# Kernel optimization log

Measured on AMD Instinct MI355X. Metric: run time of the kernel, lower is better.

The kernel has to match this reference:

```python
import jax, jax.numpy as jnp
import numpy as np

K = 3  # kernel_size per dim
DIM = 3
NUM_K = K ** DIM  # 27
# the 2^3 corner offsets of the linear B-spline support
OFFS = np.array([[(s >> d) & 1 for d in range(DIM)] for s in range(2 ** DIM)], dtype=np.int32)  # [8,3]
STRIDES = np.array([K ** d for d in range(DIM)], dtype=np.int32)  # [1,3,9]


def bspline_basis(pseudo):
    """Open B-spline basis, degree 1. pseudo: [E,3] in [0,1]. Returns basis [E,8], kidx [E,8]."""
    v = pseudo * (K - 1)
    i0 = jnp.clip(jnp.floor(v), 0, K - 2)
    f = v - i0  # fractional part in [0,1]
    i0 = i0.astype(jnp.int32)
    offs = jnp.asarray(OFFS)  # [8,3]
    w = jnp.where(offs[None].astype(bool), f[:, None, :], 1.0 - f[:, None, :])  # [E,8,3]
    basis = jnp.prod(w, axis=-1)  # [E,8]
    kidx = jnp.sum((i0[:, None, :] + offs[None]) * jnp.asarray(STRIDES)[None, None, :], axis=-1)  # [E,8]
    return basis, kidx


def spline_conv(x, src, dst, pseudo, W, Wroot, b, num_nodes):
    """SplineConv (degree 1, mean aggregation, root weight + bias)."""
    cout = W.shape[-1]
    xW = jnp.einsum('nc,kco->nko', x, W)  # [N,27,Cout]
    basis, kidx = bspline_basis(pseudo)
    flat = src[:, None] * NUM_K + kidx  # [E,8]
    g = xW.reshape(-1, cout)[flat]  # [E,8,Cout] -- dominant gather
    msg = jnp.einsum('es,eso->eo', basis, g)  # [E,Cout]
    agg = jax.ops.segment_sum(msg, dst, num_segments=num_nodes)
    cnt = jax.ops.segment_sum(jnp.ones((src.shape[0],), x.dtype), dst, num_segments=num_nodes)
    return agg / jnp.maximum(cnt, 1.0)[:, None] + x @ Wroot + b


def seg_max(x, seg, num_segments):
    m = jax.ops.segment_max(x, seg, num_segments=num_segments)
    return jnp.where(jnp.isfinite(m), m, 0.0)  # empty clusters -> 0


def setup_inputs() -> dict:
    key = jax.random.key(0)
    ks = jax.random.split(key, 16)
    N, E, B = 80000, 1280000, 16
    N1, N2 = N // 2, N1 if False else (N // 2) // 2  # N1=40000, N2=20000
    N1 = N // 2
    N2 = N1 // 2
    x = jax.random.normal(ks[0], (N, 2), dtype=jnp.float32)
    edge_index = jax.random.randint(ks[1], (2, E), 0, N, dtype=jnp.int32)
    edge_attr = jax.random.uniform(ks[2], (E, 3), dtype=jnp.float32)
    batch = jnp.sort(jax.random.randint(ks[3], (N,), 0, B, dtype=jnp.int32))
    cluster1 = jax.random.randint(ks[4], (N,), 0, N1, dtype=jnp.int32)
    cluster2 = jax.random.randint(ks[5], (N1,), 0, N2, dtype=jnp.int32)
    W1 = jax.random.normal(ks[6], (NUM_K, 2, 8), dtype=jnp.float32) * 0.3
    root1 = jax.random.normal(ks[7], (2, 8), dtype=jnp.float32) * 0.3
    b1 = jnp.zeros((8,), jnp.float32)
    W2 = jax.random.normal(ks[8], (NUM_K, 8, 16), dtype=jnp.float32) * 0.2
    root2 = jax.random.normal(ks[9], (8, 16), dtype=jnp.float32) * 0.2
    b2 = jnp.zeros((16,), jnp.float32)
    fc1_w = jax.random.normal(ks[10], (16, 64), dtype=jnp.float32) * 0.2
    fc1_b = jnp.zeros((64,), jnp.float32)
    fc2_w = jax.random.normal(ks[11], (64, 1), dtype=jnp.float32) * 0.2
    fc2_b = jnp.zeros((1,), jnp.float32)
    return dict(x=x, edge_index=edge_index, edge_attr=edge_attr, batch=batch,
                cluster1=cluster1, cluster2=cluster2,
                W1=W1, root1=root1, b1=b1, W2=W2, root2=root2, b2=b2,
                fc1_w=fc1_w, fc1_b=fc1_b, fc2_w=fc2_w, fc2_b=fc2_b)


def reference(x, edge_index, edge_attr, batch, cluster1, cluster2,
              W1, root1, b1, W2, root2, b2, fc1_w, fc1_b, fc2_w, fc2_b):
    N = x.shape[0]
    N1 = cluster1.max() * 0 + cluster2.shape[0]  # static: 40000
    N1 = cluster2.shape[0]
    N2 = N1 // 2
    B = 16
    src, dst = edge_index[0], edge_index[1]
    # level 1: SplineConv + ELU
    h = jax.nn.elu(spline_conv(x, src, dst, edge_attr, W1, root1, b1, N))
    # max_pool with precomputed cluster assignment (replaces graclus)
    x1 = seg_max(h, cluster1, N1)
    batch1 = jnp.maximum(jax.ops.segment_max(batch, cluster1, num_segments=N1), 0)
    src2 = cluster1[src]
    dst2 = cluster1[dst]
    # level 2: SplineConv + ELU on coarsened graph
    h2 = jax.nn.elu(spline_conv(x1, src2, dst2, edge_attr, W2, root2, b2, N1))
    x2 = seg_max(h2, cluster2, N2)
    batch2 = jnp.maximum(jax.ops.segment_max(batch1, cluster2, num_segments=N2), 0)
    # scatter_mean over graphs
    s = jax.ops.segment_sum(x2, batch2, num_segments=B)
    c = jax.ops.segment_sum(jnp.ones((N2,), x.dtype), batch2, num_segments=B)
    g = s / jnp.maximum(c, 1.0)[:, None]  # [B,16]
    g = jax.nn.elu(g @ fc1_w + fc1_b)  # dropout is identity in eval mode
    return jax.nn.elu(g @ fc2_w + fc2_b)  # [B,1]
```

## Files before the change

### kernel.cpp

```cpp
#include <hip/hip_runtime.h>
#include <hip/hip_fp16.h>
#include <math.h>


__device__ __forceinline__ float eluf(float x) {
    return x > 0.f ? x : (expf(x) - 1.f);
}

__device__ __forceinline__ float hlo(int v) {
    __half2 h; *(int*)&h = v; return __low2float(h);
}
__device__ __forceinline__ float hhi(int v) {
    __half2 h; *(int*)&h = v; return __high2float(h);
}

typedef _Float16 half2v __attribute__((ext_vector_type(2)));

__device__ __forceinline__ half2v uash2(unsigned u) {
    half2v h; *(unsigned*)&h = u; return h;
}

__device__ __forceinline__ float dot2f(half2v a, half2v b, float c) {
#if __has_builtin(__builtin_amdgcn_fdot2)
    return __builtin_amdgcn_fdot2(a, b, c, false);
#else
    return c + (float)a[0] * (float)b[0] + (float)a[1] * (float)b[1];
#endif
}

#define W1_STRIDE 20
#define W2H_STRIDE 68


__global__ __launch_bounds__(256) void hist_kernel(
    const int* __restrict__ ei, const int* __restrict__ cluster1,
    const int* __restrict__ cluster2,
    int* __restrict__ deg, int* __restrict__ rank,
    int* __restrict__ cdeg, int* __restrict__ rankC,
    int* __restrict__ c2deg, int* __restrict__ rank2,
    int E, int N, int N1)
{
    int i = blockIdx.x * 256 + threadIdx.x;
    if (i < E)  rank[i]  = atomicAdd(&deg[ei[E + i]], 1);
    if (i < N)  rankC[i] = atomicAdd(&cdeg[cluster1[i]], 1);
    if (i < N1) rank2[i] = atomicAdd(&c2deg[cluster2[i]], 1);
}

#define SCAN_CHUNK 4096

__global__ __launch_bounds__(256) void scan_one(
    const int* __restrict__ in0, int* __restrict__ out0, int* __restrict__ st0, int L0, int nb0,
    const int* __restrict__ in1, int* __restrict__ out1, int* __restrict__ st1, int L1, int nb1,
    const int* __restrict__ in2, int* __restrict__ out2, int* __restrict__ st2, int L2)
{
    int b = blockIdx.x;
    const int* in; int* out; int* st; int L;
    if (b < nb0)            { in = in0; out = out0; st = st0; L = L0; }
    else if (b < nb0 + nb1) { b -= nb0; in = in1; out = out1; st = st1; L = L1; }
    else                    { b -= nb0 + nb1; in = in2; out = out2; st = st2; L = L2; }
    int nb = (L + SCAN_CHUNK - 1) / SCAN_CHUNK;

    __shared__ int ls[256];
    __shared__ int pre[32];
    __shared__ int blkExcl;
    int t = threadIdx.x;
    int base = b * SCAN_CHUNK + t * 16;
    int v[16];
    int s = 0;
#pragma unroll
    for (int j = 0; j < 16; ++j) {
        int val = (base + j < L) ? in[base + j] : 0;
        v[j] = s;
        s += val;
    }
    ls[t] = s;
    __syncthreads();
    for (int off = 1; off < 256; off <<= 1) {
        int tv = (t >= off) ? ls[t - off] : 0;
        __syncthreads();
        ls[t] += tv;
        __syncthreads();
    }
    int excl = ls[t] - s;
    int total = ls[255];
    if (t == 255) {
        __threadfence();
        atomicExch(&st[b], total + 1);
    }
    if (t < b) {
        int val;
        do { val = atomicAdd(&st[t], 0); } while (val == 0);
        pre[t] = val - 1;
    }
    __syncthreads();
    if (t == 0) {
        int r = 0;
        for (int j = 0; j < b; ++j) r += pre[j];
        blkExcl = r;
    }
    __syncthreads();
    int be = blkExcl;
#pragma unroll
    for (int j = 0; j < 16; ++j)
        if (base + j < L) out[base + j] = be + excl + v[j];
    if (b == nb - 1 && t == 255) out[L] = be + total;
}

__global__ __launch_bounds__(256) void scatB_kernel(
    const int* __restrict__ ei, const float* __restrict__ attr,
    const int* __restrict__ cluster1, const int* __restrict__ cluster2,
    const float2* __restrict__ x, const float* __restrict__ W1,
    const int* __restrict__ doffs, const int* __restrict__ rank,
    const int* __restrict__ coff, const int* __restrict__ rankC,
    const int* __restrict__ c2off, const int* __restrict__ rank2,
    int* __restrict__ nidx, int* __restrict__ n1idx,
    int4* __restrict__ rec4, int E, int N, int N1)
{
    __shared__ float lw[27 * W1_STRIDE];
    for (int i = threadIdx.x; i < 27 * 16; i += 256)
        lw[(i >> 4) * W1_STRIDE + (i & 15)] = W1[i];
    __syncthreads();

    int i = blockIdx.x * 256 + threadIdx.x;
    if (i < E) {
        int s = ei[i], d = ei[E + i];
        int p = doffs[d] + rank[i];

        float vx = attr[3 * i] * 2.f, vy = attr[3 * i + 1] * 2.f, vz = attr[3 * i + 2] * 2.f;
        float ix = fmaxf(fminf(floorf(vx), 1.f), 0.f);
        float iy = fmaxf(fminf(floorf(vy), 1.f), 0.f);
        float iz = fmaxf(fminf(floorf(vz), 1.f), 0.f);
        float fx = vx - ix, fy = vy - iy, fz = vz - iz;
        int ibase = (int)ix + 3 * (int)iy + 9 * (int)iz;

        float2 xv = x[s];
        float wxv[2] = {1.f - fx, fx}, wyv[2] = {1.f - fy, fy}, wzv[2] = {1.f - fz, fz};
        float m[8];
#pragma unroll
        for (int o = 0; o < 8; ++o) m[o] = 0.f;
#pragma unroll
        for (int j = 0; j < 8; ++j) {
            int cx = j & 1, cy = (j >> 1) & 1, cz = j >> 2;
            float w = wxv[cx] * wyv[cy] * wzv[cz];
            const float* Wk = &lw[(ibase + cx + 3 * cy + 9 * cz) * W1_STRIDE];
            float a = w * xv.x, bb = w * xv.y;
            const float4 wa0 = *(const float4*)&Wk[0];
            const float4 wa1 = *(const float4*)&Wk[4];
            const float4 wb0 = *(const float4*)&Wk[8];
            const float4 wb1 = *(const float4*)&Wk[12];
            m[0] += a * wa0.x + bb * wb0.x;
            m[1] += a * wa0.y + bb * wb0.y;
            m[2] += a * wa0.z + bb * wb0.z;
            m[3] += a * wa0.w + bb * wb0.w;
            m[4] += a * wa1.x + bb * wb1.x;
            m[5] += a * wa1.y + bb * wb1.y;
            m[6] += a * wa1.z + bb * wb1.z;
            m[7] += a * wa1.w + bb * wb1.w;
        }

        unsigned hfx = __half_as_ushort(__float2half_rn(fx));
        unsigned hfy = __half_as_ushort(__float2half_rn(fy));
        unsigned hfz = __half_as_ushort(__float2half_rn(fz));
        int s2 = cluster1[s];
        int4 ra = make_int4(s2 | (ibase << 16),
                            (int)(hfx | (hfy << 16)), (int)hfz, d);
        __half2 h01 = __floats2half2_rn(m[0], m[1]);
        __half2 h23 = __floats2half2_rn(m[2], m[3]);
        __half2 h45 = __floats2half2_rn(m[4], m[5]);
        __half2 h67 = __floats2half2_rn(m[6], m[7]);
        int4 rb = make_int4(*(int*)&h01, *(int*)&h23, *(int*)&h45, *(int*)&h67);
        rec4[2 * (size_t)p]     = ra;
        rec4[2 * (size_t)p + 1] = rb;
    }
    if (i < N)  nidx[coff[cluster1[i]] + rankC[i]] = i;
    if (i < N1) n1idx[c2off[cluster2[i]] + rank2[i]] = i;
}

__global__ __launch_bounds__(256) void reduce1_kernel(
    const int* __restrict__ doffs, const unsigned short* __restrict__ recU,
    float* __restrict__ M1, int N)
{
    int lane = threadIdx.x & 63;
    int ch = lane & 7, q = lane >> 3;
    int d = (blockIdx.x << 2) + (threadIdx.x >> 6);
    if (d >= N) return;
    int beg = doffs[d], end = doffs[d + 1];
    float acc = 0.f;
    for (int p = beg + q; p < end; p += 8)
        acc += __half2float(__ushort_as_half(recU[(size_t)p * 16 + 8 + ch]));
    acc += __shfl_xor(acc, 8);
    acc += __shfl_xor(acc, 16);
    acc += __shfl_xor(acc, 32);
    if (q == 0)
        M1[(size_t)d * 8 + ch] = acc / fmaxf((float)(end - beg), 1.f);
}

__global__ __launch_bounds__(256) void node1_kernel(
    const int* __restrict__ coff, const int* __restrict__ nidx,
    const float* __restrict__ M1, const float2* __restrict__ x,
    const float* __restrict__ root1, const float* __restrict__ b1,
    const int* __restrict__ batch,
    float* __restrict__ x1c, unsigned short* __restrict__ x1chU,
    int* __restrict__ batch1, int N1)
{
    int t = blockIdx.x * 256 + threadIdx.x;
    if (t >= N1 * 8) return;
    int c = t >> 3, ch = t & 7;
    int cb = coff[c], ce = coff[c + 1];
    float r0 = root1[ch], r1 = root1[8 + ch], bo = b1[ch];
    float hm = -INFINITY;
    int bm = 0;
    for (int idx = cb; idx < ce; ++idx) {
        int d = nidx[idx];
        float2 xv = x[d];
        float h = eluf(M1[d * 8 + ch] + xv.x * r0 + xv.y * r1 + bo);
        hm = fmaxf(hm, h);
        bm = max(bm, batch[d]);
    }
    if (ce == cb) hm = 0.f;
    x1c[t] = hm;
    x1chU[t] = __half_as_ushort(__float2half_rn(hm));
    if (ch == 0) batch1[c] = bm;
}

__global__ __launch_bounds__(256) void edge2m_kernel(
    const int4* __restrict__ rec4, const unsigned short* __restrict__ x1chU,
    const float* __restrict__ W2, unsigned short* __restrict__ msg2h, int E)
{
    __shared__ unsigned lwh[27 * W2H_STRIDE];
    for (int i = threadIdx.x; i < 27 * 64; i += 256) {
        int k = i >> 6, r = i & 63;
        int o = r >> 2, c2 = r & 3;
        float a = W2[(k * 8 + 2 * c2) * 16 + o];
        float b = W2[(k * 8 + 2 * c2 + 1) * 16 + o];
        __half2 h = __floats2half2_rn(a, b);
        lwh[k * W2H_STRIDE + r] = *(unsigned*)&h;
    }
    __syncthreads();

    int t = blockIdx.x * 256 + threadIdx.x;
    if (t >= E * 4) return;
    int p = t >> 2, oq = t & 3;
    int4 m = rec4[2 * (size_t)p];
    int s2 = m.x & 0xFFFF;
    int ibase = (m.x >> 16) & 31;
    float fx = hlo(m.y), fy = hhi(m.y), fz = hlo(m.z);

    const uint4 xv4 = *(const uint4*)&x1chU[(size_t)s2 * 8];
    half2v xh0 = uash2(xv4.x), xh1 = uash2(xv4.y),
           xh2 = uash2(xv4.z), xh3 = uash2(xv4.w);

    float wx0 = 1.f - fx, wy0 = 1.f - fy, wz0 = 1.f - fz;
    float acc0 = 0.f, acc1 = 0.f, acc2 = 0.f, acc3 = 0.f;
#pragma unroll
    for (int j = 0; j < 8; ++j) {
        int cx = j & 1, cy = (j >> 1) & 1, cz = j >> 2;
        float w = (cx ? fx : wx0) * (cy ? fy : wy0) * (cz ? fz : wz0);
        int k = ibase + cx + 3 * cy + 9 * cz;
        const unsigned* base = &lwh[k * W2H_STRIDE + oq * 16];
        uint4 v0 = *(const uint4*)(base);
        uint4 v1 = *(const uint4*)(base + 4);
        uint4 v2 = *(const uint4*)(base + 8);
        uint4 v3 = *(const uint4*)(base + 12);
        float s0 = dot2f(xh0, uash2(v0.x), dot2f(xh1, uash2(v0.y),
                   dot2f(xh2, uash2(v0.z), dot2f(xh3, uash2(v0.w), 0.f))));
        float s1 = dot2f(xh0, uash2(v1.x), dot2f(xh1, uash2(v1.y),
                   dot2f(xh2, uash2(v1.z), dot2f(xh3, uash2(v1.w), 0.f))));
        float s2v = dot2f(xh0, uash2(v2.x), dot2f(xh1, uash2(v2.y),
                    dot2f(xh2, uash2(v2.z), dot2f(xh3, uash2(v2.w), 0.f))));
        float s3 = dot2f(xh0, uash2(v3.x), dot2f(xh1, uash2(v3.y),
                   dot2f(xh2, uash2(v3.z), dot2f(xh3, uash2(v3.w), 0.f))));
        acc0 = fmaf(w, s0, acc0);
        acc1 = fmaf(w, s1, acc1);
        acc2 = fmaf(w, s2v, acc2);
        acc3 = fmaf(w, s3, acc3);
    }
    __half2 lo = __floats2half2_rn(acc0, acc1);
    __half2 hi = __floats2half2_rn(acc2, acc3);
    uint2 outv = make_uint2(*(unsigned*)&lo, *(unsigned*)&hi);
    *(uint2*)&msg2h[(size_t)p * 16 + oq * 4] = outv;
}

__global__ __launch_bounds__(256) void reduce2_kernel(
    const int* __restrict__ coff, const int* __restrict__ nidx,
    const int* __restrict__ doffs, const unsigned short* __restrict__ msg2h,
    float* __restrict__ M2, int N1)
{
    int lane = threadIdx.x & 63;
    int o = lane & 15, q = lane >> 4;
    int c = (blockIdx.x << 2) + (threadIdx.x >> 6);
    if (c >= N1) return;
    int cb = coff[c], ce = coff[c + 1];
    float acc = 0.f;
    int cnt = 0;
    for (int idx = cb; idx < ce; ++idx) {
        int d = nidx[idx];
        int beg = doffs[d], end = doffs[d + 1];
        cnt += end - beg;
        for (int p = beg + q; p < end; p += 4)
            acc += __half2float(__ushort_as_half(msg2h[(size_t)p * 16 + o]));
    }
    acc += __shfl_xor(acc, 16);
    acc += __shfl_xor(acc, 32);
    if (q == 0) M2[(size_t)c * 16 + o] = acc / fmaxf((float)cnt, 1.f);
}

__global__ __launch_bounds__(256) void node2_kernel(
    const int* __restrict__ c2off, const int* __restrict__ n1idx,
    const float* __restrict__ M2, const float* __restrict__ x1c,
    const float* __restrict__ root2, const float* __restrict__ b2,
    const int* __restrict__ batch1,
    float* __restrict__ gsum, float* __restrict__ gcnt, int N2)
{
    __shared__ float ls[16 * 16];
    __shared__ float lc[16];
    for (int i = threadIdx.x; i < 256; i += 256) ls[i] = 0.f;
    if (threadIdx.x < 16) lc[threadIdx.x] = 0.f;
    __syncthreads();

    int c2 = blockIdx.x * 256 + threadIdx.x;
    if (c2 < N2) {
        int cb = c2off[c2], ce = c2off[c2 + 1];
        float hm[16];
#pragma unroll
        for (int o = 0; o < 16; ++o) hm[o] = -INFINITY;
        int bm = 0;
        for (int idx = cb; idx < ce; ++idx) {
            int n1 = n1idx[idx];
            const float4* xr4 = (const float4*)&x1c[(size_t)n1 * 8];
            float4 xa = xr4[0], xb = xr4[1];
            float xr[8] = {xa.x, xa.y, xa.z, xa.w, xb.x, xb.y, xb.z, xb.w};
#pragma unroll
            for (int o = 0; o < 16; ++o) {
                float v = M2[(size_t)n1 * 16 + o] + b2[o];
#pragma unroll
                for (int c8 = 0; c8 < 8; ++c8) v += xr[c8] * root2[c8 * 16 + o];
                hm[o] = fmaxf(hm[o], eluf(v));
            }
            bm = max(bm, batch1[n1]);
        }
        if (ce == cb) {
#pragma unroll
            for (int o = 0; o < 16; ++o) hm[o] = 0.f;
        }
#pragma unroll
        for (int o = 0; o < 16; ++o) atomicAdd(&ls[bm * 16 + o], hm[o]);
        atomicAdd(&lc[bm], 1.f);
    }
    __syncthreads();
    for (int i = threadIdx.x; i < 256; i += 256) unsafeAtomicAdd(&gsum[i], ls[i]);
    if (threadIdx.x < 16) unsafeAtomicAdd(&gcnt[threadIdx.x], lc[threadIdx.x]);
}

__global__ __launch_bounds__(256) void head_kernel(
    const float* __restrict__ gsum, const float* __restrict__ gcnt,
    const float* __restrict__ fc1_w, const float* __restrict__ fc1_b,
    const float* __restrict__ fc2_w, const float* __restrict__ fc2_b,
    float* __restrict__ out, int B)
{
    __shared__ float g[16 * 16];
    __shared__ float h1[16 * 64];
    int t = threadIdx.x;
    if (t < B * 16) {
        int b = t >> 4;
        g[t] = gsum[t] / fmaxf(gcnt[b], 1.f);
    }
    __syncthreads();
    for (int j = t; j < B * 64; j += 256) {
        int b = j >> 6, jj = j & 63;
        float s = fc1_b[jj];
#pragma unroll
        for (int c = 0; c < 16; ++c) s += g[b * 16 + c] * fc1_w[c * 64 + jj];
        h1[j] = eluf(s);
    }
    __syncthreads();
    if (t < B) {
        float s = fc2_b[0];
#pragma unroll
        for (int j = 0; j < 64; ++j) s += h1[t * 64 + j] * fc2_w[j];
        out[t] = eluf(s);
    }
}

extern "C" void kernel_launch(void* const* d_in, const int* in_sizes, int n_in,
                              void* d_out, int out_size, void* d_ws, size_t ws_size,
                              hipStream_t stream)
{
    const float* x        = (const float*)d_in[0];
    const int*   ei       = (const int*)  d_in[1];
    const float* attr     = (const float*)d_in[2];
    const int*   batch    = (const int*)  d_in[3];
    const int*   cluster1 = (const int*)  d_in[4];
    const int*   cluster2 = (const int*)  d_in[5];
    const float* W1       = (const float*)d_in[6];
    const float* root1    = (const float*)d_in[7];
    const float* b1       = (const float*)d_in[8];
    const float* W2       = (const float*)d_in[9];
    const float* root2    = (const float*)d_in[10];
    const float* b2       = (const float*)d_in[11];
    const float* fc1_w    = (const float*)d_in[12];
    const float* fc1_b    = (const float*)d_in[13];
    const float* fc2_w    = (const float*)d_in[14];
    const float* fc2_b    = (const float*)d_in[15];

    const int N  = in_sizes[0] / 2;
    const int E  = in_sizes[1] / 2;
    const int N1 = in_sizes[5];
    const int N2 = N1 / 2;
    const int B  = out_size;

    const int nb0 = (N  + SCAN_CHUNK - 1) / SCAN_CHUNK;
    const int nb1 = (N1 + SCAN_CHUNK - 1) / SCAN_CHUNK;
    const int nb2 = (N2 + SCAN_CHUNK - 1) / SCAN_CHUNK;

    int* wi = (int*)d_ws;
    size_t off = 0;
    auto alloc = [&](size_t n, size_t align = 1) {
        off = (off + align - 1) & ~(align - 1);
        size_t r = off; off += n; return r;
    };
    int*   deg    = wi + alloc(N);
    int*   cdeg   = wi + alloc(N1);
    int*   c2deg  = wi + alloc(N2);
    float* gsum   = (float*)(wi + alloc((size_t)B * 16));
    float* gcnt   = (float*)(wi + alloc(B));
    int*   st0    = wi + alloc(32);
    int*   st1    = wi + alloc(32);
    int*   st2    = wi + alloc(32);
    const size_t zcount = off;
    int*   doffs  = wi + alloc(N + 1);
    int*   coff   = wi + alloc(N1 + 1);
    int*   c2off  = wi + alloc(N2 + 1);
    int*   rank   = wi + alloc(E);
    int*   rankC  = wi + alloc(N);
    int*   rank2  = wi + alloc(N1);
    int*   nidx   = wi + alloc(N);
    int*   n1idx  = wi + alloc(N1);
    int4*  rec4   = (int4*)(wi + alloc((size_t)E * 8, 8));
    unsigned short* msg2h = (unsigned short*)(wi + alloc((size_t)E * 8, 4));
    float* M1     = (float*)(wi + alloc((size_t)N * 8, 4));
    float* x1c    = (float*)(wi + alloc((size_t)N1 * 8, 4));
    unsigned short* x1chU = (unsigned short*)(wi + alloc((size_t)N1 * 4, 4));
    int*   batch1 = wi + alloc(N1);
    float* M2     = (float*)(wi + alloc((size_t)N1 * 16, 4));
    (void)ws_size;

    hipMemsetAsync(d_ws, 0, zcount * sizeof(int), stream);

    const int eb = (E + 255) / 256;
    hist_kernel<<<eb, 256, 0, stream>>>(ei, cluster1, cluster2,
                                        deg, rank, cdeg, rankC, c2deg, rank2, E, N, N1);
    scan_one<<<nb0 + nb1 + nb2, 256, 0, stream>>>(deg, doffs, st0, N, nb0,
                                                  cdeg, coff, st1, N1, nb1,
                                                  c2deg, c2off, st2, N2);
    scatB_kernel<<<eb, 256, 0, stream>>>(ei, attr, cluster1, cluster2,
                                         (const float2*)x, W1,
                                         doffs, rank, coff, rankC, c2off, rank2,
                                         nidx, n1idx, rec4, E, N, N1);
    reduce1_kernel<<<(N + 3) / 4, 256, 0, stream>>>(
        doffs, (const unsigned short*)rec4, M1, N);
    node1_kernel<<<(N1 * 8 + 255) / 256, 256, 0, stream>>>(
        coff, nidx, M1, (const float2*)x, root1, b1, batch,
        x1c, x1chU, batch1, N1);
    edge2m_kernel<<<(E * 4 + 255) / 256, 256, 0, stream>>>(
        rec4, x1chU, W2, msg2h, E);
    reduce2_kernel<<<(N1 + 3) / 4, 256, 0, stream>>>(
        coff, nidx, doffs, msg2h, M2, N1);
    node2_kernel<<<(N2 + 255) / 256, 256, 0, stream>>>(
        c2off, n1idx, M2, x1c, root2, b2, batch1, gsum, gcnt, N2);
    head_kernel<<<1, 256, 0, stream>>>(gsum, gcnt, fc1_w, fc1_b, fc2_w, fc2_b,
                                       (float*)d_out, B);
}
```

Measured before the change: 347.9 us.

## Accumulate basis-weighted inputs per node before applying W2, dropping per-edge messages

The level-2 spline conv now reorders the algebra. Each destination node accumulates the basis-weighted source features into a 27x8 vector Y in registers and shared memory, then multiplies by W2 once per node, instead of computing a 16-wide message per edge. This removes the per-edge msg2h buffer write and reread, and most of the per-edge dot products. The cost is per-edge work spread over 64 lanes with mostly zero weights, plus a new per-node intermediate M2n. A separate comb2 kernel averages M2n per cluster, and node2 is reworked to one thread per output channel with root2 staged in shared memory.

```diff
diff --git a/kernel.cpp b/kernel.cpp
--- a/kernel.cpp
+++ b/kernel.cpp
@@ -14,22 +14,15 @@
     __half2 h; *(int*)&h = v; return __high2float(h);
 }
 
-typedef _Float16 half2v __attribute__((ext_vector_type(2)));
-
-__device__ __forceinline__ half2v uash2(unsigned u) {
-    half2v h; *(unsigned*)&h = u; return h;
-}
-
-__device__ __forceinline__ float dot2f(half2v a, half2v b, float c) {
-#if __has_builtin(__builtin_amdgcn_fdot2)
-    return __builtin_amdgcn_fdot2(a, b, c, false);
-#else
-    return c + (float)a[0] * (float)b[0] + (float)a[1] * (float)b[1];
-#endif
+__device__ __forceinline__ float hlou(unsigned v) {
+    __half2 h; *(unsigned*)&h = v; return __low2float(h);
+}
+__device__ __forceinline__ float hhiu(unsigned v) {
+    __half2 h; *(unsigned*)&h = v; return __high2float(h);
 }
 
 #define W1_STRIDE 20
-#define W2H_STRIDE 68
+#define W2T_STRIDE 217
 
 
 __global__ __launch_bounds__(256) void hist_kernel(
@@ -223,89 +216,93 @@
     if (ch == 0) batch1[c] = bm;
 }
 
-__global__ __launch_bounds__(256) void edge2m_kernel(
-    const int4* __restrict__ rec4, const unsigned short* __restrict__ x1chU,
-    const float* __restrict__ W2, unsigned short* __restrict__ msg2h, int E)
-{
-    __shared__ unsigned lwh[27 * W2H_STRIDE];
-    for (int i = threadIdx.x; i < 27 * 64; i += 256) {
-        int k = i >> 6, r = i & 63;
-        int o = r >> 2, c2 = r & 3;
-        float a = W2[(k * 8 + 2 * c2) * 16 + o];
-        float b = W2[(k * 8 + 2 * c2 + 1) * 16 + o];
-        __half2 h = __floats2half2_rn(a, b);
-        lwh[k * W2H_STRIDE + r] = *(unsigned*)&h;
-    }
-    __syncthreads();
-
+__global__ __launch_bounds__(256) void edge2Y_kernel(
+    const int* __restrict__ doffs, const int4* __restrict__ rec4,
+    const unsigned short* __restrict__ x1chU, const float* __restrict__ W2,
+    float* __restrict__ M2n, int N)
+{
+    __shared__ float w2t[16 * W2T_STRIDE];
+    __shared__ float Y[4 * 256];
+    int tid = threadIdx.x;
+    for (int j = tid; j < 27 * 8 * 16; j += 256) {
+        int o = j & 15, kc = j >> 4;
+        w2t[o * W2T_STRIDE + kc] = W2[j];
+    }
+    int wid = tid >> 6, lane = tid & 63;
+    int d = (blockIdx.x << 2) + wid;
+    float* Yw = &Y[wid * 256];
+
+    int myk = lane >> 1;
+    int csel = lane & 1;
+    float y0 = 0.f, y1 = 0.f, y2 = 0.f, y3 = 0.f;
+    if (d < N) {
+        int beg = doffs[d], end = doffs[d + 1];
+        for (int p = beg; p < end; ++p) {
+            int4 ra = rec4[2 * (size_t)p];
+            int s2 = ra.x & 0xFFFF;
+            int ibase = (ra.x >> 16) & 31;
+            float fx = hlo(ra.y), fy = hhi(ra.y), fz = hlo(ra.z);
+            const uint4 xv4 = *(const uint4*)&x1chU[(size_t)s2 * 8];
+            unsigned lo_ = csel ? xv4.z : xv4.x;
+            unsigned hi_ = csel ? xv4.w : xv4.y;
+            float xa = hlou(lo_), xb = hhiu(lo_);
+            float xc = hlou(hi_), xd = hhiu(hi_);
+            int tt = myk - ibase;
+            float w = 0.f;
+            if (tt >= 0 && tt <= 13 && ((13851 >> tt) & 1)) {
+                int dxm = tt % 3;
+                int rem = tt / 3;
+                int dym = rem % 3;
+                int dzm = rem / 3;
+                float wx = dxm ? fx : 1.f - fx;
+                float wy = dym ? fy : 1.f - fy;
+                float wz = dzm ? fz : 1.f - fz;
+                w = wx * wy * wz;
+            }
+            y0 = fmaf(w, xa, y0);
+            y1 = fmaf(w, xb, y1);
+            y2 = fmaf(w, xc, y2);
+            y3 = fmaf(w, xd, y3);
+        }
+    }
+    *(float4*)&Yw[lane * 4] = make_float4(y0, y1, y2, y3);
+    __syncthreads();
+
+    if (d < N) {
+        int o = lane & 15, q = lane >> 4;
+        const float* wrow = &w2t[o * W2T_STRIDE];
+        float acc = 0.f;
+#pragma unroll 6
+        for (int i = 0; i < 54; ++i) {
+            int kc = 4 * i + q;
+            acc = fmaf(wrow[kc], Yw[kc], acc);
+        }
+        acc += __shfl_xor(acc, 16);
+        acc += __shfl_xor(acc, 32);
+        if (q == 0) M2n[(size_t)d * 16 + o] = acc;
+    }
+}
+
+__global__ __launch_bounds__(256) void comb2_kernel(
+    const int* __restrict__ coff, const int* __restrict__ nidx,
+    const int* __restrict__ doffs, const float* __restrict__ M2n,
+    float* __restrict__ M2, int N1)
+{
     int t = blockIdx.x * 256 + threadIdx.x;
-    if (t >= E * 4) return;
-    int p = t >> 2, oq = t & 3;
-    int4 m = rec4[2 * (size_t)p];
-    int s2 = m.x & 0xFFFF;
-    int ibase = (m.x >> 16) & 31;
-    float fx = hlo(m.y), fy = hhi(m.y), fz = hlo(m.z);
-
-    const uint4 xv4 = *(const uint4*)&x1chU[(size_t)s2 * 8];
-    half2v xh0 = uash2(xv4.x), xh1 = uash2(xv4.y),
-           xh2 = uash2(xv4.z), xh3 = uash2(xv4.w);
-
-    float wx0 = 1.f - fx, wy0 = 1.f - fy, wz0 = 1.f - fz;
-    float acc0 = 0.f, acc1 = 0.f, acc2 = 0.f, acc3 = 0.f;
-#pragma unroll
-    for (int j = 0; j < 8; ++j) {
-        int cx = j & 1, cy = (j >> 1) & 1, cz = j >> 2;
-        float w = (cx ? fx : wx0) * (cy ? fy : wy0) * (cz ? fz : wz0);
-        int k = ibase + cx + 3 * cy + 9 * cz;
-        const unsigned* base = &lwh[k * W2H_STRIDE + oq * 16];
-        uint4 v0 = *(const uint4*)(base);
-        uint4 v1 = *(const uint4*)(base + 4);
-        uint4 v2 = *(const uint4*)(base + 8);
-        uint4 v3 = *(const uint4*)(base + 12);
-        float s0 = dot2f(xh0, uash2(v0.x), dot2f(xh1, uash2(v0.y),
-                   dot2f(xh2, uash2(v0.z), dot2f(xh3, uash2(v0.w), 0.f))));
-        float s1 = dot2f(xh0, uash2(v1.x), dot2f(xh1, uash2(v1.y),
-                   dot2f(xh2, uash2(v1.z), dot2f(xh3, uash2(v1.w), 0.f))));
-        float s2v = dot2f(xh0, uash2(v2.x), dot2f(xh1, uash2(v2.y),
-                    dot2f(xh2, uash2(v2.z), dot2f(xh3, uash2(v2.w), 0.f))));
-        float s3 = dot2f(xh0, uash2(v3.x), dot2f(xh1, uash2(v3.y),
-                   dot2f(xh2, uash2(v3.z), dot2f(xh3, uash2(v3.w), 0.f))));
-        acc0 = fmaf(w, s0, acc0);
-        acc1 = fmaf(w, s1, acc1);
-        acc2 = fmaf(w, s2v, acc2);
-        acc3 = fmaf(w, s3, acc3);
-    }
-    __half2 lo = __floats2half2_rn(acc0, acc1);
-    __half2 hi = __floats2half2_rn(acc2, acc3);
-    uint2 outv = make_uint2(*(unsigned*)&lo, *(unsigned*)&hi);
-    *(uint2*)&msg2h[(size_t)p * 16 + oq * 4] = outv;
-}
-
-__global__ __launch_bounds__(256) void reduce2_kernel(
-    const int* __restrict__ coff, const int* __restrict__ nidx,
-    const int* __restrict__ doffs, const unsigned short* __restrict__ msg2h,
-    float* __restrict__ M2, int N1)
-{
-    int lane = threadIdx.x & 63;
-    int o = lane & 15, q = lane >> 4;
-    int c = (blockIdx.x << 2) + (threadIdx.x >> 6);
-    if (c >= N1) return;
+    if (t >= N1 * 16) return;
+    int c = t >> 4, o = t & 15;
     int cb = coff[c], ce = coff[c + 1];
     float acc = 0.f;
     int cnt = 0;
     for (int idx = cb; idx < ce; ++idx) {
         int d = nidx[idx];
-        int beg = doffs[d], end = doffs[d + 1];
-        cnt += end - beg;
-        for (int p = beg + q; p < end; p += 4)
-            acc += __half2float(__ushort_as_half(msg2h[(size_t)p * 16 + o]));
-    }
-    acc += __shfl_xor(acc, 16);
-    acc += __shfl_xor(acc, 32);
-    if (q == 0) M2[(size_t)c * 16 + o] = acc / fmaxf((float)cnt, 1.f);
-}
-
-__global__ __launch_bounds__(256) void node2_kernel(
+        acc += M2n[(size_t)d * 16 + o];
+        cnt += doffs[d + 1] - doffs[d];
+    }
+    M2[t] = acc / fmaxf((float)cnt, 1.f);
+}
+
+__global__ __launch_bounds__(256) void node2f_kernel(
     const int* __restrict__ c2off, const int* __restrict__ n1idx,
     const float* __restrict__ M2, const float* __restrict__ x1c,
     const float* __restrict__ root2, const float* __restrict__ b2,
@@ -314,38 +311,34 @@
 {
     __shared__ float ls[16 * 16];
     __shared__ float lc[16];
+    __shared__ float r2[128];
     for (int i = threadIdx.x; i < 256; i += 256) ls[i] = 0.f;
     if (threadIdx.x < 16) lc[threadIdx.x] = 0.f;
-    __syncthreads();
-
-    int c2 = blockIdx.x * 256 + threadIdx.x;
-    if (c2 < N2) {
+    if (threadIdx.x < 128) r2[threadIdx.x] = root2[threadIdx.x];
+    __syncthreads();
+
+    int t = blockIdx.x * 256 + threadIdx.x;
+    if (t < N2 * 16) {
+        int c2 = t >> 4, o = t & 15;
         int cb = c2off[c2], ce = c2off[c2 + 1];
-        float hm[16];
-#pragma unroll
-        for (int o = 0; o < 16; ++o) hm[o] = -INFINITY;
+        float bo = b2[o];
+        float hm = -INFINITY;
         int bm = 0;
         for (int idx = cb; idx < ce; ++idx) {
             int n1 = n1idx[idx];
             const float4* xr4 = (const float4*)&x1c[(size_t)n1 * 8];
             float4 xa = xr4[0], xb = xr4[1];
-            float xr[8] = {xa.x, xa.y, xa.z, xa.w, xb.x, xb.y, xb.z, xb.w};
-#pragma unroll
-            for (int o = 0; o < 16; ++o) {
-                float v = M2[(size_t)n1 * 16 + o] + b2[o];
-#pragma unroll
-                for (int c8 = 0; c8 < 8; ++c8) v += xr[c8] * root2[c8 * 16 + o];
-                hm[o] = fmaxf(hm[o], eluf(v));
-            }
+            float v = M2[(size_t)n1 * 16 + o] + bo
+                    + xa.x * r2[o] + xa.y * r2[16 + o]
+                    + xa.z * r2[32 + o] + xa.w * r2[48 + o]
+                    + xb.x * r2[64 + o] + xb.y * r2[80 + o]
+                    + xb.z * r2[96 + o] + xb.w * r2[112 + o];
+            hm = fmaxf(hm, eluf(v));
             bm = max(bm, batch1[n1]);
         }
-        if (ce == cb) {
-#pragma unroll
-            for (int o = 0; o < 16; ++o) hm[o] = 0.f;
-        }
-#pragma unroll
-        for (int o = 0; o < 16; ++o) atomicAdd(&ls[bm * 16 + o], hm[o]);
-        atomicAdd(&lc[bm], 1.f);
+        if (ce == cb) hm = 0.f;
+        atomicAdd(&ls[bm * 16 + o], hm);
+        if (o == 0) atomicAdd(&lc[bm], 1.f);
     }
     __syncthreads();
     for (int i = threadIdx.x; i < 256; i += 256) unsafeAtomicAdd(&gsum[i], ls[i]);
@@ -437,8 +430,8 @@
     int*   nidx   = wi + alloc(N);
     int*   n1idx  = wi + alloc(N1);
     int4*  rec4   = (int4*)(wi + alloc((size_t)E * 8, 8));
-    unsigned short* msg2h = (unsigned short*)(wi + alloc((size_t)E * 8, 4));
     float* M1     = (float*)(wi + alloc((size_t)N * 8, 4));
+    float* M2n    = (float*)(wi + alloc((size_t)N * 16, 4));
     float* x1c    = (float*)(wi + alloc((size_t)N1 * 8, 4));
     unsigned short* x1chU = (unsigned short*)(wi + alloc((size_t)N1 * 4, 4));
     int*   batch1 = wi + alloc(N1);
@@ -462,11 +455,11 @@
     node1_kernel<<<(N1 * 8 + 255) / 256, 256, 0, stream>>>(
         coff, nidx, M1, (const float2*)x, root1, b1, batch,
         x1c, x1chU, batch1, N1);
-    edge2m_kernel<<<(E * 4 + 255) / 256, 256, 0, stream>>>(
-        rec4, x1chU, W2, msg2h, E);
-    reduce2_kernel<<<(N1 + 3) / 4, 256, 0, stream>>>(
-        coff, nidx, doffs, msg2h, M2, N1);
-    node2_kernel<<<(N2 + 255) / 256, 256, 0, stream>>>(
+    edge2Y_kernel<<<(N + 3) / 4, 256, 0, stream>>>(
+        doffs, rec4, x1chU, W2, M2n, N);
+    comb2_kernel<<<(N1 * 16 + 255) / 256, 256, 0, stream>>>(
+        coff, nidx, doffs, M2n, M2, N1);
+    node2f_kernel<<<(N2 * 16 + 255) / 256, 256, 0, stream>>>(
         c2off, n1idx, M2, x1c, root2, b2, batch1, gsum, gcnt, N2);
     head_kernel<<<1, 256, 0, stream>>>(gsum, gcnt, fc1_w, fc1_b, fc2_w, fc2_b,
                                        (float*)d_out, B);
```

Result: slower. 429.9 us (+23.6%).
